# Performance work log

Measured on AMD Instinct MI355X. Metric: run time of the kernel, lower is better.

The kernel has to match this reference:

```python
import jax, jax.numpy as jnp
import numpy as np

N_S = 50000
N_T = 50000
E = 1600000
IN_C = 128
HID_C = 128
OUT_C = 64


def _sage_conv(x_src, x_dst, edge_index, W_l, W_r, b, n_dst):
    """PyG bipartite SAGEConv, aggr='mean': lin_l(mean_j x_src[j]) + lin_r(x_dst).
    lin_l has bias, lin_r does not."""
    row, col = edge_index[0], edge_index[1]
    msg = x_src[row]                                          # [E, F_in] gather
    summed = jax.ops.segment_sum(msg, col, num_segments=n_dst)  # [n_dst, F_in]
    cnt = jax.ops.segment_sum(jnp.ones((row.shape[0],), x_src.dtype), col,
                              num_segments=n_dst)
    mean = summed / jnp.maximum(cnt, 1.0)[:, None]            # zero for isolated nodes
    return mean @ W_l + b + x_dst @ W_r


def setup_inputs() -> dict:
    key = jax.random.key(0)
    ks = jax.random.split(key, 20)
    x_s = jax.random.normal(ks[0], (N_S, IN_C), dtype=jnp.float32)
    x_t = jax.random.normal(ks[1], (N_T, IN_C), dtype=jnp.float32)
    s2t = jnp.stack([jax.random.randint(ks[2], (E,), 0, N_S),
                     jax.random.randint(ks[3], (E,), 0, N_T)])
    t2s = jnp.stack([jax.random.randint(ks[4], (E,), 0, N_T),
                     jax.random.randint(ks[5], (E,), 0, N_S)])

    def lin(k, fi, fo):
        return jax.random.normal(k, (fi, fo), dtype=jnp.float32) / np.sqrt(fi)

    return {
        'x_s': x_s, 'x_t': x_t, 's2t': s2t, 't2s': t2s,
        'W1s_l': lin(ks[6], IN_C, HID_C), 'W1s_r': lin(ks[7], IN_C, HID_C),
        'b1s': jnp.zeros((HID_C,), jnp.float32),
        'W1t_l': lin(ks[8], IN_C, HID_C), 'W1t_r': lin(ks[9], IN_C, HID_C),
        'b1t': jnp.zeros((HID_C,), jnp.float32),
        'W2s_l': lin(ks[10], HID_C, OUT_C), 'W2s_r': lin(ks[11], HID_C, OUT_C),
        'b2s': jnp.zeros((OUT_C,), jnp.float32),
        'W2t_l': lin(ks[12], HID_C, OUT_C), 'W2t_r': lin(ks[13], HID_C, OUT_C),
        'b2t': jnp.zeros((OUT_C,), jnp.float32),
    }


def reference(x_s, x_t, s2t, t2s,
              W1s_l, W1s_r, b1s, W1t_l, W1t_r, b1t,
              W2s_l, W2s_r, b2s, W2t_l, W2t_r, b2t):
    # layer 1 (cross-side message passing)
    x_new_s = _sage_conv(x_t, x_s, t2s, W1s_l, W1s_r, b1s, N_S)
    x_new_t = _sage_conv(x_s, x_t, s2t, W1t_l, W1t_r, b1t, N_T)
    # layer 2
    z_s = _sage_conv(x_new_t, x_new_s, t2s, W2s_l, W2s_r, b2s, N_S)
    z_t = _sage_conv(x_new_s, x_new_t, s2t, W2t_l, W2t_r, b2t, N_T)
    return (z_s, z_t)
```

## Files before the change

kernel.cpp:

```cpp
#include <hip/hip_runtime.h>

typedef unsigned int u32;
typedef unsigned short u16;
typedef __attribute__((ext_vector_type(4))) float f32x4;
typedef __attribute__((ext_vector_type(2))) float f32x2;
typedef __attribute__((ext_vector_type(8))) short bf16x8;

static inline int cdiv(int a, int b) { return (a + b - 1) / b; }

#define NBKT 512
#define BSHIFT 7
#define BNODES 128
#define EPB2 16384
#define CAP 5120

__device__ inline u32 pk_bf16(float a, float b) {
  u32 ua = __builtin_bit_cast(u32, a);
  ua += 0x7fffu + ((ua >> 16) & 1u);
  u32 ub = __builtin_bit_cast(u32, b);
  ub += 0x7fffu + ((ub >> 16) & 1u);
  return (ua >> 16) | (ub & 0xffff0000u);
}

__global__ __launch_bounds__(256) void cvt_f8_k(const float* __restrict__ xs,
                                                const float* __restrict__ xt,
                                                int n4S, int n4T,
                                                u32* __restrict__ xsf8,
                                                u32* __restrict__ xtf8) {
  int i = blockIdx.x * 256 + threadIdx.x;
  const float* src;
  u32* dst;
  int q;
  if (i < n4S) {
    src = xs; dst = xsf8; q = i;
  } else {
    q = i - n4S;
    if (q >= n4T) return;
    src = xt; dst = xtf8;
  }
  float4 v = *reinterpret_cast<const float4*>(src + (size_t)q * 4);
  u32 p = 0;
  p = __builtin_amdgcn_cvt_pk_fp8_f32(v.x, v.y, p, false);
  p = __builtin_amdgcn_cvt_pk_fp8_f32(v.z, v.w, p, true);
  dst[q] = p;
}

__global__ __launch_bounds__(256) void cvtW_k(const float* __restrict__ W1sl,
                                              const float* __restrict__ W1sr,
                                              const float* __restrict__ W1tl,
                                              const float* __restrict__ W1tr,
                                              const float* __restrict__ W2A_s,
                                              const float* __restrict__ W2B_s,
                                              const float* __restrict__ W2A_t,
                                              const float* __restrict__ W2B_t,
                                              u16* __restrict__ out) {
  int seg = blockIdx.x * 256 + threadIdx.x;
  if (seg >= 12288) return;
  const float* W;
  int ncol, base, local;
  if (seg < 8192) {
    int m = seg >> 11; local = seg & 2047; ncol = 128; base = m * 16384;
    W = m == 0 ? W1sl : m == 1 ? W1sr : m == 2 ? W1tl : W1tr;
  } else {
    int m = (seg - 8192) >> 10; local = (seg - 8192) & 1023; ncol = 64; base = 65536 + m * 8192;
    W = m == 0 ? W2A_s : m == 1 ? W2B_s : m == 2 ? W2A_t : W2B_t;
  }
  int col = local >> 4;
  int k0 = (local & 15) * 8;
  u16 tmp[8];
#pragma unroll
  for (int e = 0; e < 8; ++e) {
    float v = W[(size_t)(k0 + e) * ncol + col];
    tmp[e] = (u16)(pk_bf16(v, 0.f) & 0xffffu);
  }
  *reinterpret_cast<uint4*>(out + (size_t)base + col * 128 + k0) =
      *reinterpret_cast<uint4*>(tmp);
}


__global__ __launch_bounds__(512) void scatfuse2_k(const int* __restrict__ rowS,
                                                   const int* __restrict__ colS,
                                                   const int* __restrict__ rowT,
                                                   const int* __restrict__ colT,
                                                   int E, int nblk,
                                                   int* __restrict__ gcur,
                                                   u32* __restrict__ bktS,
                                                   u32* __restrict__ bktT) {
  __shared__ u32 stage[EPB2];
  __shared__ int h[NBKT], lstart[NBKT], lpos[NBKT], gbase[NBKT];
  int b = blockIdx.x;
  const int *row, *col;
  u32* bkt;
  int* gc;
  if (b < nblk) {
    row = rowS; col = colS; bkt = bktS; gc = gcur;
  } else {
    b -= nblk; row = rowT; col = colT; bkt = bktT; gc = gcur + NBKT;
  }
  int t = threadIdx.x;
  h[t] = 0;
  __syncthreads();
  int base = b * EPB2, end = min(base + EPB2, E);
  for (int i = base + t; i < end; i += 512) atomicAdd(&h[col[i] >> BSHIFT], 1);
  __syncthreads();
  lstart[t] = h[t];
  __syncthreads();
  for (int off = 1; off < NBKT; off <<= 1) {
    int x = (t >= off) ? lstart[t - off] : 0;
    __syncthreads();
    if (t >= off) lstart[t] += x;
    __syncthreads();
  }
  {
    int hc = h[t];
    int ls = lstart[t] - hc;
    lstart[t] = ls;
    lpos[t] = ls;
    gbase[t] = hc ? atomicAdd(&gc[t], hc) : 0;
  }
  __syncthreads();
  for (int i = base + t; i < end; i += 512) {
    int c = col[i];
    int p = atomicAdd(&lpos[c >> BSHIFT], 1);
    stage[p] = ((u32)row[i] << 16) | (u32)c;
  }
  __syncthreads();
  int total = end - base;
  for (int j = t; j < total; j += 512) {
    u32 v = stage[j];
    u32 d = v & 0xffffu;
    int bi = d >> BSHIFT;
    int gp = gbase[bi] + (j - lstart[bi]);
    bkt[(size_t)bi * CAP + gp] = ((v >> 16) << BSHIFT) | (d & (BNODES - 1));
  }
}


__global__ __launch_bounds__(256) void sortb_k(u32* __restrict__ bktS,
                                               u32* __restrict__ bktT,
                                               const int* __restrict__ gcur,
                                               int NS, int NT,
                                               u32* __restrict__ stdegS,
                                               u32* __restrict__ stdegT) {
  __shared__ u32 srcs[CAP];
  __shared__ int cnt[BNODES], excl[BNODES], st[BNODES], cur[BNODES];
  int nbkS = (NS + BNODES - 1) >> BSHIFT;
  int b = blockIdx.x;
  u32 *bkt, *stdeg;
  int N, ec;
  if (b < nbkS) {
    bkt = bktS + (size_t)b * CAP; ec = gcur[b]; stdeg = stdegS; N = NS;
  } else {
    b -= nbkS;
    bkt = bktT + (size_t)b * CAP; ec = gcur[NBKT + b]; stdeg = stdegT; N = NT;
  }
  int node0 = b << BSHIFT;
  int t = threadIdx.x;
  if (t < BNODES) cnt[t] = 0;
  __syncthreads();
  for (int i = t; i < ec; i += 256) atomicAdd(&cnt[bkt[i] & (BNODES - 1)], 1);
  __syncthreads();
  if (t < BNODES) excl[t] = cnt[t];
  __syncthreads();
  for (int off = 1; off < BNODES; off <<= 1) {
    int x = 0;
    if (t < BNODES && t >= off) x = excl[t - off];
    __syncthreads();
    if (t < BNODES && t >= off) excl[t] += x;
    __syncthreads();
  }
  if (t < BNODES) {
    int s0 = excl[t] - cnt[t];
    st[t] = s0;
    cur[t] = s0;
  }
  __syncthreads();
  for (int i = t; i < ec; i += 256) {
    u32 p = bkt[i];
    int ps = atomicAdd(&cur[p & (BNODES - 1)], 1);
    srcs[ps] = p >> BSHIFT;
  }
  __syncthreads();
  for (int i = t; i < ec; i += 256) bkt[i] = srcs[i];
  if (t < BNODES) {
    int node = node0 + t;
    if (node < N) stdeg[node] = ((u32)st[t] << 16) | (u32)cnt[t];
  }
}


__global__ __launch_bounds__(256) void agg128D_k(const u32* __restrict__ xs_f8,
                                                 const u32* __restrict__ xt_f8,
                                                 const u32* __restrict__ bktS,
                                                 const u32* __restrict__ bktT,
                                                 const u32* __restrict__ stdegS,
                                                 const u32* __restrict__ stdegT,
                                                 int NS, int NT,
                                                 u32* __restrict__ mean_s,
                                                 u32* __restrict__ mean_t) {
  int nbS = (NS + 15) >> 4;
  int nbT = (NT + 15) >> 4;
  int slot = blockIdx.x & 7;
  int pair = blockIdx.x >> 3;
  int gid = threadIdx.x >> 4, fl = threadIdx.x & 15;
  const u32 *xf8, *bkt, *stdeg;
  u32* outm;
  int N, node;
  if (slot < 4) {
    int blk = pair * 4 + slot;
    if (blk >= nbS) return;
    xf8 = xt_f8; bkt = bktS; stdeg = stdegS; outm = mean_s; N = NS;
    node = blk * 16 + gid;
  } else {
    int blk = pair * 4 + (slot - 4);
    if (blk >= nbT) return;
    xf8 = xs_f8; bkt = bktT; stdeg = stdegT; outm = mean_t; N = NT;
    node = blk * 16 + gid;
  }
  if (node >= N) return;
  u32 sd = stdeg[node];
  int deg = (int)(sd & 0xffffu);
  const u32* csr = bkt + (size_t)(node >> BSHIFT) * CAP + (sd >> 16);
  f32x2 a0 = {0.f, 0.f}, a1 = {0.f, 0.f}, a2 = {0.f, 0.f}, a3 = {0.f, 0.f};
  int i = 0;
  for (; i + 8 <= deg; i += 8) {
    int c[8];
#pragma unroll
    for (int j = 0; j < 8; ++j) c[j] = csr[i + j];
    uint2 v[8];
#pragma unroll
    for (int j = 0; j < 8; ++j)
      v[j] = *reinterpret_cast<const uint2*>(xf8 + (size_t)c[j] * 32 + fl * 2);
#pragma unroll
    for (int j = 0; j < 8; ++j) {
      a0 += __builtin_amdgcn_cvt_pk_f32_fp8(v[j].x, false);
      a1 += __builtin_amdgcn_cvt_pk_f32_fp8(v[j].x, true);
      a2 += __builtin_amdgcn_cvt_pk_f32_fp8(v[j].y, false);
      a3 += __builtin_amdgcn_cvt_pk_f32_fp8(v[j].y, true);
    }
  }
  for (; i + 4 <= deg; i += 4) {
    int c[4];
#pragma unroll
    for (int j = 0; j < 4; ++j) c[j] = csr[i + j];
    uint2 v[4];
#pragma unroll
    for (int j = 0; j < 4; ++j)
      v[j] = *reinterpret_cast<const uint2*>(xf8 + (size_t)c[j] * 32 + fl * 2);
#pragma unroll
    for (int j = 0; j < 4; ++j) {
      a0 += __builtin_amdgcn_cvt_pk_f32_fp8(v[j].x, false);
      a1 += __builtin_amdgcn_cvt_pk_f32_fp8(v[j].x, true);
      a2 += __builtin_amdgcn_cvt_pk_f32_fp8(v[j].y, false);
      a3 += __builtin_amdgcn_cvt_pk_f32_fp8(v[j].y, true);
    }
  }
  for (; i < deg; ++i) {
    int c0 = csr[i];
    uint2 v0 = *reinterpret_cast<const uint2*>(xf8 + (size_t)c0 * 32 + fl * 2);
    a0 += __builtin_amdgcn_cvt_pk_f32_fp8(v0.x, false);
    a1 += __builtin_amdgcn_cvt_pk_f32_fp8(v0.x, true);
    a2 += __builtin_amdgcn_cvt_pk_f32_fp8(v0.y, false);
    a3 += __builtin_amdgcn_cvt_pk_f32_fp8(v0.y, true);
  }
  float inv = deg > 0 ? 1.f / (float)deg : 0.f;
  uint4 p;
  p.x = pk_bf16(a0.x * inv, a0.y * inv);
  p.y = pk_bf16(a1.x * inv, a1.y * inv);
  p.z = pk_bf16(a2.x * inv, a2.y * inv);
  p.w = pk_bf16(a3.x * inv, a3.y * inv);
  *reinterpret_cast<uint4*>(outm + (size_t)node * 64 + fl * 4) = p;
}


__global__ __launch_bounds__(256) void agg64D_k(const u32* __restrict__ hs_f8,
                                                const u32* __restrict__ ht_f8,
                                                const u32* __restrict__ bktS,
                                                const u32* __restrict__ bktT,
                                                const u32* __restrict__ stdegS,
                                                const u32* __restrict__ stdegT,
                                                int NS, int NT,
                                                const float* __restrict__ g_s,
                                                const float* __restrict__ g_t,
                                                const float* __restrict__ b2s,
                                                const float* __restrict__ b2t,
                                                float* __restrict__ z_s,
                                                float* __restrict__ z_t) {
  int nbS = (NS + 15) >> 4;
  int nbT = (NT + 15) >> 4;
  int slot = blockIdx.x & 7;
  int pair = blockIdx.x >> 3;
  int gid = threadIdx.x >> 4, fl = threadIdx.x & 15;
  const u32 *hf8, *bkt, *stdeg;
  const float *g, *bias;
  float* z;
  int N, node;
  if (slot < 4) {
    int blk = pair * 4 + slot;
    if (blk >= nbS) return;
    hf8 = ht_f8; bkt = bktS; stdeg = stdegS; g = g_s; bias = b2s; z = z_s; N = NS;
    node = blk * 16 + gid;
  } else {
    int blk = pair * 4 + (slot - 4);
    if (blk >= nbT) return;
    hf8 = hs_f8; bkt = bktT; stdeg = stdegT; g = g_t; bias = b2t; z = z_t; N = NT;
    node = blk * 16 + gid;
  }
  if (node >= N) return;
  u32 sd = stdeg[node];
  int deg = (int)(sd & 0xffffu);
  const u32* csr = bkt + (size_t)(node >> BSHIFT) * CAP + (sd >> 16);
  f32x2 a0 = {0.f, 0.f}, a1 = {0.f, 0.f};
  int i = 0;
  for (; i + 8 <= deg; i += 8) {
    int c[8];
#pragma unroll
    for (int j = 0; j < 8; ++j) c[j] = csr[i + j];
    u32 v[8];
#pragma unroll
    for (int j = 0; j < 8; ++j) v[j] = hf8[(size_t)c[j] * 16 + fl];
#pragma unroll
    for (int j = 0; j < 8; ++j) {
      a0 += __builtin_amdgcn_cvt_pk_f32_fp8(v[j], false);
      a1 += __builtin_amdgcn_cvt_pk_f32_fp8(v[j], true);
    }
  }
  for (; i + 4 <= deg; i += 4) {
    int c[4];
#pragma unroll
    for (int j = 0; j < 4; ++j) c[j] = csr[i + j];
    u32 v[4];
#pragma unroll
    for (int j = 0; j < 4; ++j) v[j] = hf8[(size_t)c[j] * 16 + fl];
#pragma unroll
    for (int j = 0; j < 4; ++j) {
      a0 += __builtin_amdgcn_cvt_pk_f32_fp8(v[j], false);
      a1 += __builtin_amdgcn_cvt_pk_f32_fp8(v[j], true);
    }
  }
  for (; i < deg; ++i) {
    u32 v0 = hf8[(size_t)csr[i] * 16 + fl];
    a0 += __builtin_amdgcn_cvt_pk_f32_fp8(v0, false);
    a1 += __builtin_amdgcn_cvt_pk_f32_fp8(v0, true);
  }
  float inv = deg > 0 ? 1.f / (float)deg : 0.f;
  float4 gv = *reinterpret_cast<const float4*>(g + (size_t)node * 64 + fl * 4);
  float4 bv = *reinterpret_cast<const float4*>(bias + fl * 4);
  float4 r;
  r.x = a0.x * inv + gv.x + bv.x;
  r.y = a0.y * inv + gv.y + bv.y;
  r.z = a1.x * inv + gv.z + bv.z;
  r.w = a1.y * inv + gv.w + bv.w;
  *reinterpret_cast<float4*>(z + (size_t)node * 64 + fl * 4) = r;
}


__global__ __launch_bounds__(256) void gemm1_dual_k(
    const u16* __restrict__ mean_s, const float* __restrict__ xs,
    const u16* __restrict__ mean_t, const float* __restrict__ xt,
    const u16* __restrict__ Wt_s0, const u16* __restrict__ Wt_s1,
    const u16* __restrict__ Wt_t0, const u16* __restrict__ Wt_t1,
    const float* __restrict__ b1s, const float* __restrict__ b1t,
    u16* __restrict__ xnew_s, u16* __restrict__ xnew_t, int NS, int NT) {
  int nb1 = (NS + 127) >> 7;
  int b = blockIdx.x;
  const u16 *A0, *Wt0, *Wt1;
  const float *X1, *bias;
  u16* out;
  int M, rowBase;
  if (b < nb1) {
    A0 = mean_s; X1 = xs; Wt0 = Wt_s0; Wt1 = Wt_s1; bias = b1s; out = xnew_s;
    M = NS; rowBase = b * 128;
  } else {
    A0 = mean_t; X1 = xt; Wt0 = Wt_t0; Wt1 = Wt_t1; bias = b1t; out = xnew_t;
    M = NT; rowBase = (b - nb1) * 128;
  }
  const int lane = threadIdx.x & 63;
  const int wid = threadIdx.x >> 6;
  const int r16 = lane & 15;
  const int kg = lane >> 4;
  rowBase += wid * 32;

  f32x4 acc[2][8];
#pragma unroll
  for (int i = 0; i < 2; ++i)
#pragma unroll
    for (int j = 0; j < 8; ++j) acc[i][j] = (f32x4){0.f, 0.f, 0.f, 0.f};

  const int r0 = min(rowBase + r16, M - 1);
  const int r1 = min(rowBase + 16 + r16, M - 1);

#pragma unroll
  for (int ch = 0; ch < 8; ++ch) {
    const int koff = (ch & 3) * 32 + kg * 8;
    bf16x8 x0, x1;
    if (ch < 4) {
      x0 = *reinterpret_cast<const bf16x8*>(A0 + (size_t)r0 * 128 + koff);
      x1 = *reinterpret_cast<const bf16x8*>(A0 + (size_t)r1 * 128 + koff);
    } else {
      float4 fa = *reinterpret_cast<const float4*>(X1 + (size_t)r0 * 128 + koff);
      float4 fb = *reinterpret_cast<const float4*>(X1 + (size_t)r0 * 128 + koff + 4);
      uint4 u0;
      u0.x = pk_bf16(fa.x, fa.y); u0.y = pk_bf16(fa.z, fa.w);
      u0.z = pk_bf16(fb.x, fb.y); u0.w = pk_bf16(fb.z, fb.w);
      x0 = __builtin_bit_cast(bf16x8, u0);
      float4 fc = *reinterpret_cast<const float4*>(X1 + (size_t)r1 * 128 + koff);
      float4 fd = *reinterpret_cast<const float4*>(X1 + (size_t)r1 * 128 + koff + 4);
      uint4 u1;
      u1.x = pk_bf16(fc.x, fc.y); u1.y = pk_bf16(fc.z, fc.w);
      u1.z = pk_bf16(fd.x, fd.y); u1.w = pk_bf16(fd.z, fd.w);
      x1 = __builtin_bit_cast(bf16x8, u1);
    }
    const u16* Wt = (ch < 4) ? Wt0 : Wt1;
#pragma unroll
    for (int cb = 0; cb < 8; ++cb) {
      bf16x8 w = *reinterpret_cast<const bf16x8*>(Wt + (size_t)(cb * 16 + r16) * 128 + koff);
      acc[0][cb] = __builtin_amdgcn_mfma_f32_16x16x32_bf16(w, x0, acc[0][cb], 0, 0, 0);
      acc[1][cb] = __builtin_amdgcn_mfma_f32_16x16x32_bf16(w, x1, acc[1][cb], 0, 0, 0);
    }
  }

#pragma unroll
  for (int cb = 0; cb < 8; ++cb) {
    float4 bv = *reinterpret_cast<const float4*>(bias + cb * 16 + kg * 4);
#pragma unroll
    for (int rb = 0; rb < 2; ++rb) {
      int row = rowBase + rb * 16 + r16;
      if (row < M) {
        f32x4 a = acc[rb][cb];
        uint2 p;
        p.x = pk_bf16(a[0] + bv.x, a[1] + bv.y);
        p.y = pk_bf16(a[2] + bv.z, a[3] + bv.w);
        *reinterpret_cast<uint2*>(out + (size_t)row * 128 + cb * 16 + kg * 4) = p;
      }
    }
  }
}


__global__ __launch_bounds__(256) void gemm2_dual_k(
    const u16* __restrict__ xnew_s, const u16* __restrict__ xnew_t,
    const u16* __restrict__ WtA_s, const u16* __restrict__ WtB_s,
    const u16* __restrict__ WtA_t, const u16* __restrict__ WtB_t,
    u32* __restrict__ hs_f8, u32* __restrict__ ht_f8,
    float* __restrict__ g_s, float* __restrict__ g_t, int NS, int NT) {
  int nb1 = (NS + 127) >> 7;
  int b = blockIdx.x;
  const u16 *X, *WtA, *WtB;
  u32* h;
  float* g;
  int M, rowBase;
  if (b < nb1) {
    X = xnew_s; WtA = WtA_s; WtB = WtB_s; h = hs_f8; g = g_s; M = NS; rowBase = b * 128;
  } else {
    X = xnew_t; WtA = WtA_t; WtB = WtB_t; h = ht_f8; g = g_t; M = NT;
    rowBase = (b - nb1) * 128;
  }
  const int lane = threadIdx.x & 63;
  const int wid = threadIdx.x >> 6;
  const int r16 = lane & 15;
  const int kg = lane >> 4;
  rowBase += wid * 32;

  f32x4 acc[2][8];
#pragma unroll
  for (int i = 0; i < 2; ++i)
#pragma unroll
    for (int j = 0; j < 8; ++j) acc[i][j] = (f32x4){0.f, 0.f, 0.f, 0.f};

  const int r0 = min(rowBase + r16, M - 1);
  const int r1 = min(rowBase + 16 + r16, M - 1);

#pragma unroll
  for (int ch = 0; ch < 4; ++ch) {
    const int koff = ch * 32 + kg * 8;
    bf16x8 x0 = *reinterpret_cast<const bf16x8*>(X + (size_t)r0 * 128 + koff);
    bf16x8 x1 = *reinterpret_cast<const bf16x8*>(X + (size_t)r1 * 128 + koff);
#pragma unroll
    for (int cb = 0; cb < 8; ++cb) {
      const u16* Wt = (cb < 4) ? WtA : WtB;
      bf16x8 w = *reinterpret_cast<const bf16x8*>(Wt + (size_t)((cb & 3) * 16 + r16) * 128 + koff);
      acc[0][cb] = __builtin_amdgcn_mfma_f32_16x16x32_bf16(w, x0, acc[0][cb], 0, 0, 0);
      acc[1][cb] = __builtin_amdgcn_mfma_f32_16x16x32_bf16(w, x1, acc[1][cb], 0, 0, 0);
    }
  }

#pragma unroll
  for (int cb = 0; cb < 8; ++cb) {
#pragma unroll
    for (int rb = 0; rb < 2; ++rb) {
      int row = rowBase + rb * 16 + r16;
      if (row < M) {
        f32x4 a = acc[rb][cb];
        if (cb < 4) {
          u32 p = 0;
          p = __builtin_amdgcn_cvt_pk_fp8_f32(a[0], a[1], p, false);
          p = __builtin_amdgcn_cvt_pk_fp8_f32(a[2], a[3], p, true);
          h[(size_t)row * 16 + cb * 4 + kg] = p;
        } else {
          *reinterpret_cast<f32x4*>(g + (size_t)row * 64 + (cb - 4) * 16 + kg * 4) = a;
        }
      }
    }
  }
}


extern "C" void kernel_launch(void* const* d_in, const int* in_sizes, int n_in,
                              void* d_out, int out_size, void* d_ws, size_t ws_size,
                              hipStream_t stream) {
  const float* x_s = (const float*)d_in[0];
  const float* x_t = (const float*)d_in[1];
  const int* s2t = (const int*)d_in[2];
  const int* t2s = (const int*)d_in[3];
  const float* W1s_l = (const float*)d_in[4];
  const float* W1s_r = (const float*)d_in[5];
  const float* b1s = (const float*)d_in[6];
  const float* W1t_l = (const float*)d_in[7];
  const float* W1t_r = (const float*)d_in[8];
  const float* b1t = (const float*)d_in[9];
  const float* W2s_l = (const float*)d_in[10];
  const float* W2s_r = (const float*)d_in[11];
  const float* b2s = (const float*)d_in[12];
  const float* W2t_l = (const float*)d_in[13];
  const float* W2t_r = (const float*)d_in[14];
  const float* b2t = (const float*)d_in[15];

  const int NS = in_sizes[0] / 128;
  const int NT = in_sizes[1] / 128;
  const int E = in_sizes[2] / 2;

  char* ws = (char*)d_ws;
  size_t off = 0;
  auto alloc = [&](size_t bytes) -> void* {
    void* p = ws + off;
    off = (off + bytes + 255) & ~(size_t)255;
    return p;
  };

  const int nbkS = cdiv(NS, BNODES);
  const int nbkT = cdiv(NT, BNODES);
  const int nblk2 = cdiv(E, EPB2);

  int* gcur = (int*)alloc(2 * NBKT * 4);
  u16* Wt = (u16*)alloc(98304 * 2);
  u32* bktS = (u32*)alloc((size_t)nbkS * CAP * 4);
  u32* bktT = (u32*)alloc((size_t)nbkT * CAP * 4);
  u32* stdegS = (u32*)alloc((size_t)NS * 4);
  u32* stdegT = (u32*)alloc((size_t)NT * 4);

  char* R2 = (char*)alloc((size_t)(NS + NT) * 512);
  u16* xnew_s = (u16*)alloc((size_t)(NS + NT) * 256);
  u16* xnew_t = xnew_s + (size_t)NS * 128;

  u16* mean_s = (u16*)R2;
  u16* mean_t = mean_s + (size_t)NS * 128;
  u32* hs_f8 = (u32*)R2;
  u32* ht_f8 = hs_f8 + (size_t)NS * 16;
  float* g_s = (float*)(ht_f8 + (size_t)NT * 16);
  float* g_t = g_s + (size_t)NS * 64;

  u32* xs_f8 = (u32*)(R2 + (size_t)(NS + NT) * 384);
  u32* xt_f8 = xs_f8 + (size_t)NS * 32;

  u16* Wt1s_l = Wt;
  u16* Wt1s_r = Wt + 16384;
  u16* Wt1t_l = Wt + 32768;
  u16* Wt1t_r = Wt + 49152;
  u16* Wt2A_s = Wt + 65536;
  u16* Wt2B_s = Wt + 73728;
  u16* Wt2A_t = Wt + 81920;
  u16* Wt2B_t = Wt + 90112;

  float* z_s = (float*)d_out;
  float* z_t = (float*)d_out + (size_t)NS * 64;

  cvt_f8_k<<<cdiv(NS * 32 + NT * 32, 256), 256, 0, stream>>>(
      x_s, x_t, NS * 32, NT * 32, xs_f8, xt_f8);
  cvtW_k<<<48, 256, 0, stream>>>(W1s_l, W1s_r, W1t_l, W1t_r,
                                 W2t_l, W2s_r, W2s_l, W2t_r, Wt);
  hipMemsetAsync(gcur, 0, 2 * NBKT * 4, stream);

  scatfuse2_k<<<2 * nblk2, 512, 0, stream>>>(t2s, t2s + E, s2t, s2t + E, E, nblk2,
                                             gcur, bktS, bktT);
  sortb_k<<<nbkS + nbkT, 256, 0, stream>>>(bktS, bktT, gcur, NS, NT, stdegS, stdegT);

  const int npair128 = cdiv(max(cdiv(NS, 16), cdiv(NT, 16)), 4);

  agg128D_k<<<npair128 * 8, 256, 0, stream>>>(
      xs_f8, xt_f8, bktS, bktT, stdegS, stdegT, NS, NT, (u32*)mean_s, (u32*)mean_t);
  gemm1_dual_k<<<cdiv(NS, 128) + cdiv(NT, 128), 256, 0, stream>>>(
      mean_s, x_s, mean_t, x_t, Wt1s_l, Wt1s_r, Wt1t_l, Wt1t_r,
      b1s, b1t, xnew_s, xnew_t, NS, NT);

  gemm2_dual_k<<<cdiv(NS, 128) + cdiv(NT, 128), 256, 0, stream>>>(
      xnew_s, xnew_t, Wt2A_s, Wt2B_s, Wt2A_t, Wt2B_t, hs_f8, ht_f8, g_s, g_t, NS, NT);
  agg64D_k<<<npair128 * 8, 256, 0, stream>>>(
      hs_f8, ht_f8, bktS, bktT, stdegS, stdegT, NS, NT,
      g_s, g_t, b2s, b2t, z_s, z_t);
}
```

Measured before the change: 220.4 us.

## Pre-convert inputs to bf16 and widen GEMM row tiles to 64 rows per wave

The input conversion kernel now also writes bf16 copies of x_s and x_t, so gemm1 reads half the bytes and skips in-loop fp32-to-bf16 packing. Both dual GEMMs move to 256-row blocks with 64 rows per wave, split into two column halves, so each weight fragment load feeds four MFMAs instead of two. The scatter edges-per-block constant is also halved to launch more scatter blocks. The cost is an extra bf16 buffer written in the conversion pass, and fewer GEMM blocks in flight.

```diff
diff --git a/kernel.cpp b/kernel.cpp
--- a/kernel.cpp
+++ b/kernel.cpp
@@ -11,7 +11,7 @@
 #define NBKT 512
 #define BSHIFT 7
 #define BNODES 128
-#define EPB2 16384
+#define EPB2 8192
 #define CAP 5120
 
 __device__ inline u32 pk_bf16(float a, float b) {
@@ -22,27 +22,34 @@
   return (ua >> 16) | (ub & 0xffff0000u);
 }
 
-__global__ __launch_bounds__(256) void cvt_f8_k(const float* __restrict__ xs,
+__global__ __launch_bounds__(256) void cvt_in_k(const float* __restrict__ xs,
                                                 const float* __restrict__ xt,
                                                 int n4S, int n4T,
+                                                uint2* __restrict__ xsbf,
+                                                uint2* __restrict__ xtbf,
                                                 u32* __restrict__ xsf8,
                                                 u32* __restrict__ xtf8) {
   int i = blockIdx.x * 256 + threadIdx.x;
   const float* src;
-  u32* dst;
+  uint2* obf;
+  u32* of8;
   int q;
   if (i < n4S) {
-    src = xs; dst = xsf8; q = i;
+    src = xs; obf = xsbf; of8 = xsf8; q = i;
   } else {
     q = i - n4S;
     if (q >= n4T) return;
-    src = xt; dst = xtf8;
+    src = xt; obf = xtbf; of8 = xtf8;
   }
   float4 v = *reinterpret_cast<const float4*>(src + (size_t)q * 4);
+  uint2 b;
+  b.x = pk_bf16(v.x, v.y);
+  b.y = pk_bf16(v.z, v.w);
+  obf[q] = b;
   u32 p = 0;
   p = __builtin_amdgcn_cvt_pk_fp8_f32(v.x, v.y, p, false);
   p = __builtin_amdgcn_cvt_pk_fp8_f32(v.z, v.w, p, true);
-  dst[q] = p;
+  of8[q] = p;
 }
 
 __global__ __launch_bounds__(256) void cvtW_k(const float* __restrict__ W1sl,
@@ -356,82 +363,76 @@
 
 
 __global__ __launch_bounds__(256) void gemm1_dual_k(
-    const u16* __restrict__ mean_s, const float* __restrict__ xs,
-    const u16* __restrict__ mean_t, const float* __restrict__ xt,
+    const u16* __restrict__ mean_s, const u16* __restrict__ xs_bf,
+    const u16* __restrict__ mean_t, const u16* __restrict__ xt_bf,
     const u16* __restrict__ Wt_s0, const u16* __restrict__ Wt_s1,
     const u16* __restrict__ Wt_t0, const u16* __restrict__ Wt_t1,
     const float* __restrict__ b1s, const float* __restrict__ b1t,
     u16* __restrict__ xnew_s, u16* __restrict__ xnew_t, int NS, int NT) {
-  int nb1 = (NS + 127) >> 7;
+  int nb1 = (NS + 255) >> 8;
   int b = blockIdx.x;
-  const u16 *A0, *Wt0, *Wt1;
-  const float *X1, *bias;
+  const u16 *A0, *A1, *Wt0, *Wt1;
+  const float* bias;
   u16* out;
   int M, rowBase;
   if (b < nb1) {
-    A0 = mean_s; X1 = xs; Wt0 = Wt_s0; Wt1 = Wt_s1; bias = b1s; out = xnew_s;
-    M = NS; rowBase = b * 128;
-  } else {
-    A0 = mean_t; X1 = xt; Wt0 = Wt_t0; Wt1 = Wt_t1; bias = b1t; out = xnew_t;
-    M = NT; rowBase = (b - nb1) * 128;
+    A0 = mean_s; A1 = xs_bf; Wt0 = Wt_s0; Wt1 = Wt_s1; bias = b1s; out = xnew_s;
+    M = NS; rowBase = b * 256;
+  } else {
+    A0 = mean_t; A1 = xt_bf; Wt0 = Wt_t0; Wt1 = Wt_t1; bias = b1t; out = xnew_t;
+    M = NT; rowBase = (b - nb1) * 256;
   }
   const int lane = threadIdx.x & 63;
   const int wid = threadIdx.x >> 6;
   const int r16 = lane & 15;
   const int kg = lane >> 4;
-  rowBase += wid * 32;
-
-  f32x4 acc[2][8];
-#pragma unroll
-  for (int i = 0; i < 2; ++i)
-#pragma unroll
-    for (int j = 0; j < 8; ++j) acc[i][j] = (f32x4){0.f, 0.f, 0.f, 0.f};
-
-  const int r0 = min(rowBase + r16, M - 1);
-  const int r1 = min(rowBase + 16 + r16, M - 1);
-
-#pragma unroll
-  for (int ch = 0; ch < 8; ++ch) {
-    const int koff = (ch & 3) * 32 + kg * 8;
-    bf16x8 x0, x1;
-    if (ch < 4) {
-      x0 = *reinterpret_cast<const bf16x8*>(A0 + (size_t)r0 * 128 + koff);
-      x1 = *reinterpret_cast<const bf16x8*>(A0 + (size_t)r1 * 128 + koff);
-    } else {
-      float4 fa = *reinterpret_cast<const float4*>(X1 + (size_t)r0 * 128 + koff);
-      float4 fb = *reinterpret_cast<const float4*>(X1 + (size_t)r0 * 128 + koff + 4);
-      uint4 u0;
-      u0.x = pk_bf16(fa.x, fa.y); u0.y = pk_bf16(fa.z, fa.w);
-      u0.z = pk_bf16(fb.x, fb.y); u0.w = pk_bf16(fb.z, fb.w);
-      x0 = __builtin_bit_cast(bf16x8, u0);
-      float4 fc = *reinterpret_cast<const float4*>(X1 + (size_t)r1 * 128 + koff);
-      float4 fd = *reinterpret_cast<const float4*>(X1 + (size_t)r1 * 128 + koff + 4);
-      uint4 u1;
-      u1.x = pk_bf16(fc.x, fc.y); u1.y = pk_bf16(fc.z, fc.w);
-      u1.z = pk_bf16(fd.x, fd.y); u1.w = pk_bf16(fd.z, fd.w);
-      x1 = __builtin_bit_cast(bf16x8, u1);
-    }
-    const u16* Wt = (ch < 4) ? Wt0 : Wt1;
-#pragma unroll
-    for (int cb = 0; cb < 8; ++cb) {
-      bf16x8 w = *reinterpret_cast<const bf16x8*>(Wt + (size_t)(cb * 16 + r16) * 128 + koff);
-      acc[0][cb] = __builtin_amdgcn_mfma_f32_16x16x32_bf16(w, x0, acc[0][cb], 0, 0, 0);
-      acc[1][cb] = __builtin_amdgcn_mfma_f32_16x16x32_bf16(w, x1, acc[1][cb], 0, 0, 0);
-    }
-  }
-
-#pragma unroll
-  for (int cb = 0; cb < 8; ++cb) {
-    float4 bv = *reinterpret_cast<const float4*>(bias + cb * 16 + kg * 4);
-#pragma unroll
-    for (int rb = 0; rb < 2; ++rb) {
-      int row = rowBase + rb * 16 + r16;
-      if (row < M) {
-        f32x4 a = acc[rb][cb];
-        uint2 p;
-        p.x = pk_bf16(a[0] + bv.x, a[1] + bv.y);
-        p.y = pk_bf16(a[2] + bv.z, a[3] + bv.w);
-        *reinterpret_cast<uint2*>(out + (size_t)row * 128 + cb * 16 + kg * 4) = p;
+  rowBase += wid * 64;
+
+  int r[4];
+#pragma unroll
+  for (int f = 0; f < 4; ++f) r[f] = min(rowBase + f * 16 + r16, M - 1);
+
+#pragma unroll
+  for (int cbh = 0; cbh < 2; ++cbh) {
+    f32x4 acc[4][4];
+#pragma unroll
+    for (int f = 0; f < 4; ++f)
+#pragma unroll
+      for (int j = 0; j < 4; ++j) acc[f][j] = (f32x4){0.f, 0.f, 0.f, 0.f};
+
+#pragma unroll
+    for (int ch = 0; ch < 8; ++ch) {
+      const u16* A = (ch < 4) ? A0 : A1;
+      const u16* Wt = (ch < 4) ? Wt0 : Wt1;
+      const int koff = (ch & 3) * 32 + kg * 8;
+      bf16x8 x[4];
+#pragma unroll
+      for (int f = 0; f < 4; ++f)
+        x[f] = *reinterpret_cast<const bf16x8*>(A + (size_t)r[f] * 128 + koff);
+#pragma unroll
+      for (int cb = 0; cb < 4; ++cb) {
+        int cbg = cbh * 4 + cb;
+        bf16x8 w = *reinterpret_cast<const bf16x8*>(Wt + (size_t)(cbg * 16 + r16) * 128 + koff);
+#pragma unroll
+        for (int f = 0; f < 4; ++f)
+          acc[f][cb] = __builtin_amdgcn_mfma_f32_16x16x32_bf16(w, x[f], acc[f][cb], 0, 0, 0);
+      }
+    }
+
+#pragma unroll
+    for (int cb = 0; cb < 4; ++cb) {
+      int cbg = cbh * 4 + cb;
+      float4 bv = *reinterpret_cast<const float4*>(bias + cbg * 16 + kg * 4);
+#pragma unroll
+      for (int f = 0; f < 4; ++f) {
+        int row = rowBase + f * 16 + r16;
+        if (row < M) {
+          f32x4 a = acc[f][cb];
+          uint2 p;
+          p.x = pk_bf16(a[0] + bv.x, a[1] + bv.y);
+          p.y = pk_bf16(a[2] + bv.z, a[3] + bv.w);
+          *reinterpret_cast<uint2*>(out + (size_t)row * 128 + cbg * 16 + kg * 4) = p;
+        }
       }
     }
   }
@@ -444,61 +445,68 @@
     const u16* __restrict__ WtA_t, const u16* __restrict__ WtB_t,
     u32* __restrict__ hs_f8, u32* __restrict__ ht_f8,
     float* __restrict__ g_s, float* __restrict__ g_t, int NS, int NT) {
-  int nb1 = (NS + 127) >> 7;
+  int nb1 = (NS + 255) >> 8;
   int b = blockIdx.x;
   const u16 *X, *WtA, *WtB;
   u32* h;
   float* g;
   int M, rowBase;
   if (b < nb1) {
-    X = xnew_s; WtA = WtA_s; WtB = WtB_s; h = hs_f8; g = g_s; M = NS; rowBase = b * 128;
+    X = xnew_s; WtA = WtA_s; WtB = WtB_s; h = hs_f8; g = g_s; M = NS; rowBase = b * 256;
   } else {
     X = xnew_t; WtA = WtA_t; WtB = WtB_t; h = ht_f8; g = g_t; M = NT;
-    rowBase = (b - nb1) * 128;
+    rowBase = (b - nb1) * 256;
   }
   const int lane = threadIdx.x & 63;
   const int wid = threadIdx.x >> 6;
   const int r16 = lane & 15;
   const int kg = lane >> 4;
-  rowBase += wid * 32;
-
-  f32x4 acc[2][8];
-#pragma unroll
-  for (int i = 0; i < 2; ++i)
-#pragma unroll
-    for (int j = 0; j < 8; ++j) acc[i][j] = (f32x4){0.f, 0.f, 0.f, 0.f};
-
-  const int r0 = min(rowBase + r16, M - 1);
-  const int r1 = min(rowBase + 16 + r16, M - 1);
-
-#pragma unroll
-  for (int ch = 0; ch < 4; ++ch) {
-    const int koff = ch * 32 + kg * 8;
-    bf16x8 x0 = *reinterpret_cast<const bf16x8*>(X + (size_t)r0 * 128 + koff);
-    bf16x8 x1 = *reinterpret_cast<const bf16x8*>(X + (size_t)r1 * 128 + koff);
-#pragma unroll
-    for (int cb = 0; cb < 8; ++cb) {
-      const u16* Wt = (cb < 4) ? WtA : WtB;
-      bf16x8 w = *reinterpret_cast<const bf16x8*>(Wt + (size_t)((cb & 3) * 16 + r16) * 128 + koff);
-      acc[0][cb] = __builtin_amdgcn_mfma_f32_16x16x32_bf16(w, x0, acc[0][cb], 0, 0, 0);
-      acc[1][cb] = __builtin_amdgcn_mfma_f32_16x16x32_bf16(w, x1, acc[1][cb], 0, 0, 0);
-    }
-  }
-
-#pragma unroll
-  for (int cb = 0; cb < 8; ++cb) {
-#pragma unroll
-    for (int rb = 0; rb < 2; ++rb) {
-      int row = rowBase + rb * 16 + r16;
-      if (row < M) {
-        f32x4 a = acc[rb][cb];
-        if (cb < 4) {
-          u32 p = 0;
-          p = __builtin_amdgcn_cvt_pk_fp8_f32(a[0], a[1], p, false);
-          p = __builtin_amdgcn_cvt_pk_fp8_f32(a[2], a[3], p, true);
-          h[(size_t)row * 16 + cb * 4 + kg] = p;
-        } else {
-          *reinterpret_cast<f32x4*>(g + (size_t)row * 64 + (cb - 4) * 16 + kg * 4) = a;
+  rowBase += wid * 64;
+
+  int r[4];
+#pragma unroll
+  for (int f = 0; f < 4; ++f) r[f] = min(rowBase + f * 16 + r16, M - 1);
+
+#pragma unroll
+  for (int cbh = 0; cbh < 2; ++cbh) {
+    const u16* Wt = (cbh == 0) ? WtA : WtB;
+    f32x4 acc[4][4];
+#pragma unroll
+    for (int f = 0; f < 4; ++f)
+#pragma unroll
+      for (int j = 0; j < 4; ++j) acc[f][j] = (f32x4){0.f, 0.f, 0.f, 0.f};
+
+#pragma unroll
+    for (int ch = 0; ch < 4; ++ch) {
+      const int koff = ch * 32 + kg * 8;
+      bf16x8 x[4];
+#pragma unroll
+      for (int f = 0; f < 4; ++f)
+        x[f] = *reinterpret_cast<const bf16x8*>(X + (size_t)r[f] * 128 + koff);
+#pragma unroll
+      for (int cb = 0; cb < 4; ++cb) {
+        bf16x8 w = *reinterpret_cast<const bf16x8*>(Wt + (size_t)(cb * 16 + r16) * 128 + koff);
+#pragma unroll
+        for (int f = 0; f < 4; ++f)
+          acc[f][cb] = __builtin_amdgcn_mfma_f32_16x16x32_bf16(w, x[f], acc[f][cb], 0, 0, 0);
+      }
+    }
+
+#pragma unroll
+    for (int cb = 0; cb < 4; ++cb) {
+#pragma unroll
+      for (int f = 0; f < 4; ++f) {
+        int row = rowBase + f * 16 + r16;
+        if (row < M) {
+          f32x4 a = acc[f][cb];
+          if (cbh == 0) {
+            u32 p = 0;
+            p = __builtin_amdgcn_cvt_pk_fp8_f32(a[0], a[1], p, false);
+            p = __builtin_amdgcn_cvt_pk_fp8_f32(a[2], a[3], p, true);
+            h[(size_t)row * 16 + cb * 4 + kg] = p;
+          } else {
+            *reinterpret_cast<f32x4*>(g + (size_t)row * 64 + cb * 16 + kg * 4) = a;
+          }
         }
       }
     }
@@ -552,6 +560,8 @@
   char* R2 = (char*)alloc((size_t)(NS + NT) * 512);
   u16* xnew_s = (u16*)alloc((size_t)(NS + NT) * 256);
   u16* xnew_t = xnew_s + (size_t)NS * 128;
+  u16* xs_bf = (u16*)alloc((size_t)(NS + NT) * 256);
+  u16* xt_bf = xs_bf + (size_t)NS * 128;
 
   u16* mean_s = (u16*)R2;
   u16* mean_t = mean_s + (size_t)NS * 128;
@@ -575,8 +585,8 @@
   float* z_s = (float*)d_out;
   float* z_t = (float*)d_out + (size_t)NS * 64;
 
-  cvt_f8_k<<<cdiv(NS * 32 + NT * 32, 256), 256, 0, stream>>>(
-      x_s, x_t, NS * 32, NT * 32, xs_f8, xt_f8);
+  cvt_in_k<<<cdiv(NS * 32 + NT * 32, 256), 256, 0, stream>>>(
+      x_s, x_t, NS * 32, NT * 32, (uint2*)xs_bf, (uint2*)xt_bf, xs_f8, xt_f8);
   cvtW_k<<<48, 256, 0, stream>>>(W1s_l, W1s_r, W1t_l, W1t_r,
                                  W2t_l, W2s_r, W2s_l, W2t_r, Wt);
   hipMemsetAsync(gcur, 0, 2 * NBKT * 4, stream);
@@ -589,11 +599,11 @@
 
   agg128D_k<<<npair128 * 8, 256, 0, stream>>>(
       xs_f8, xt_f8, bktS, bktT, stdegS, stdegT, NS, NT, (u32*)mean_s, (u32*)mean_t);
-  gemm1_dual_k<<<cdiv(NS, 128) + cdiv(NT, 128), 256, 0, stream>>>(
-      mean_s, x_s, mean_t, x_t, Wt1s_l, Wt1s_r, Wt1t_l, Wt1t_r,
+  gemm1_dual_k<<<cdiv(NS, 256) + cdiv(NT, 256), 256, 0, stream>>>(
+      mean_s, xs_bf, mean_t, xt_bf, Wt1s_l, Wt1s_r, Wt1t_l, Wt1t_r,
       b1s, b1t, xnew_s, xnew_t, NS, NT);
 
-  gemm2_dual_k<<<cdiv(NS, 128) + cdiv(NT, 128), 256, 0, stream>>>(
+  gemm2_dual_k<<<cdiv(NS, 256) + cdiv(NT, 256), 256, 0, stream>>>(
       xnew_s, xnew_t, Wt2A_s, Wt2B_s, Wt2A_t, Wt2B_t, hs_f8, ht_f8, g_s, g_t, NS, NT);
   agg64D_k<<<npair128 * 8, 256, 0, stream>>>(
       hs_f8, ht_f8, bktS, bktT, stdegS, stdegT, NS, NT,
```

New measurement: 195.5 us. -11.3%, faster.
